# Kernel optimization log

Hardware: AMD Instinct MI355X
Metric: run time of the kernel (lower is better)

## Reference

```python
import jax, jax.numpy as jnp
import numpy as np

MAX_REL = 64  # max_relative_position (init kwarg)


def setup_inputs() -> dict:
    B, S, D, K = 8, 2048, 256, MAX_REL
    key = jax.random.key(0)
    ks = jax.random.split(key, 12)
    scale = 0.02
    return {
        "repre": jax.random.normal(ks[0], (B, S, D), jnp.float32),
        "mask": jnp.ones((B, S), jnp.int32),
        "wq1": jax.random.normal(ks[1], (D, D), jnp.float32) * scale,
        "bq1": jnp.zeros((D,), jnp.float32),
        "wk1": jax.random.normal(ks[2], (D, D), jnp.float32) * scale,
        "bk1": jnp.zeros((D,), jnp.float32),
        "rel1": jax.random.normal(ks[3], (2 * K + 1, D), jnp.float32) * scale,
        "wq2": jax.random.normal(ks[4], (D, D), jnp.float32) * scale,
        "bq2": jnp.zeros((D,), jnp.float32),
        "wk2": jax.random.normal(ks[5], (D, D), jnp.float32) * scale,
        "bk2": jnp.zeros((D,), jnp.float32),
        "rel2": jax.random.normal(ks[6], (2 * K + 1, D), jnp.float32) * scale,
    }


def _attn_logits(x, wq, bq, wk, bk, rel_emb, invalid, rel_idx):
    # Single-head relative-position attention scores (OpenNMT style):
    # query is pre-scaled by 1/sqrt(d); relative-key bias folded into scores.
    B, S, D = x.shape
    q = (x @ wq.T + bq) / jnp.sqrt(jnp.asarray(D, x.dtype))  # [B,S,D]
    k = x @ wk.T + bk                                        # [B,S,D]
    scores = jnp.einsum("bqd,bkd->bqk", q, k)               # [B,S,S]
    # relative-position term: q . rel_emb[clip(k-q)] without the [S,S,D] table
    q_rel = jnp.einsum("bqd,rd->bqr", q, rel_emb)            # [B,S,2K+1]
    idx = jnp.broadcast_to(rel_idx[None, :, :], (B, S, S))
    rel_scores = jnp.take_along_axis(q_rel, idx, axis=2)     # [B,S,S]
    scores = scores + rel_scores
    return jnp.where(invalid, jnp.asarray(-1e18, scores.dtype), scores)


def reference(repre, mask, wq1, bq1, wk1, bk1, rel1, wq2, bq2, wk2, bk2, rel2):
    B, S, D = repre.shape
    K = MAX_REL
    pos = jnp.arange(S)
    rel_idx = jnp.clip(pos[None, :] - pos[:, None], -K, K) + K  # [S,S] in [0,2K]
    # square_mask = ~(mask^T @ mask): attend only where both positions valid
    invalid = (mask[:, :, None] * mask[:, None, :]) == 0        # [B,S,S] bool
    span_st_logits = _attn_logits(repre, wq1, bq1, wk1, bk1, rel1, invalid, rel_idx)
    span_ed_logits = _attn_logits(repre, wq2, bq2, wk2, bk2, rel2, invalid, rel_idx)
    return (span_st_logits, span_ed_logits)
```

## Files before the change

### kernel.cpp

```cpp
#include <hip/hip_runtime.h>
#include <hip/hip_bf16.h>

typedef __attribute__((ext_vector_type(4))) float f32x4;
typedef __attribute__((ext_vector_type(8))) short short8;

#define BS   8
#define SQ   2048
#define DD   256
#define KREL 64
#define NREL 129

static const size_t OFF_XBF   = 0;
static const size_t OFF_WBF   = 8388608;
static const size_t OFF_RELBF = 8912896;
static const size_t OFF_WR    = 9044992;
static const size_t OFF_CR    = 9307136;
static const size_t OFF_QK    = 9309184;
static const size_t OFF_QR    = 42863616;

struct ConvArgs {
  const float* src[7];
  __hip_bfloat16* dst[7];
  float scale[7];
  int cum4[8];
};
struct bf4 { __hip_bfloat16 a, b, c, d; };

__global__ __launch_bounds__(256) void convert_k(ConvArgs A) {
  const int idx = blockIdx.x * 256 + threadIdx.x;
  if (idx >= A.cum4[7]) return;
  int rg = 0;
  #pragma unroll
  for (int t = 1; t < 7; ++t) rg += (idx >= A.cum4[t]);
  const int local = idx - A.cum4[rg];
  const float4 v = ((const float4*)A.src[rg])[local];
  const float sc = A.scale[rg];
  bf4 o;
  o.a = __float2bfloat16(v.x * sc);
  o.b = __float2bfloat16(v.y * sc);
  o.c = __float2bfloat16(v.z * sc);
  o.d = __float2bfloat16(v.w * sc);
  ((bf4*)A.dst[rg])[local] = o;
}

__global__ __launch_bounds__(256) void wr_k(const __hip_bfloat16* __restrict__ relbf,
                                            const __hip_bfloat16* __restrict__ wbf,
                                            const float* __restrict__ bq1,
                                            const float* __restrict__ bq2,
                                            __hip_bfloat16* __restrict__ wr,
                                            float* __restrict__ cr) {
  const int r = blockIdx.x;
  const int h = blockIdx.y;
  const int e = threadIdx.x;
  const int lane = e & 63, wv = e >> 6;
  const __hip_bfloat16* rel = relbf + (size_t)h * (NREL * DD);
  const __hip_bfloat16* wq  = wbf + (size_t)h * (2 * DD * DD);
  float a0 = 0.f, a1 = 0.f, a2 = 0.f, a3 = 0.f;
  if (r < NREL) {
    #pragma unroll 4
    for (int d = 0; d < DD; d += 4) {
      a0 += __bfloat162float(rel[r * DD + d + 0]) * __bfloat162float(wq[(d + 0) * DD + e]);
      a1 += __bfloat162float(rel[r * DD + d + 1]) * __bfloat162float(wq[(d + 1) * DD + e]);
      a2 += __bfloat162float(rel[r * DD + d + 2]) * __bfloat162float(wq[(d + 2) * DD + e]);
      a3 += __bfloat162float(rel[r * DD + d + 3]) * __bfloat162float(wq[(d + 3) * DD + e]);
    }
  }
  wr[((size_t)h * DD + r) * DD + e] = __float2bfloat16((a0 + a1) + (a2 + a3));

  const float* bq = h ? bq2 : bq1;
  float p = (r < NREL) ? bq[e] * 0.0625f * __bfloat162float(rel[r * DD + e]) : 0.f;
  #pragma unroll
  for (int o = 32; o > 0; o >>= 1) p += __shfl_down(p, o, 64);
  __shared__ float wred[4];
  if (lane == 0) wred[wv] = p;
  __syncthreads();
  if (e == 0) cr[h * DD + r] = (wred[0] + wred[1]) + (wred[2] + wred[3]);
}

__device__ __forceinline__ void stage_tile(const __hip_bfloat16* __restrict__ A,
                                           const __hip_bfloat16* __restrict__ B,
                                           int rowBase, int colBase, int k0,
                                           char* As, char* Bs, int wv, int lane) {
  #pragma unroll
  for (int inst = 0; inst < 2; ++inst) {
    const int lds_off = wv * 2048 + inst * 1024;
    const int e0 = (lds_off >> 1) + lane * 8;
    const int r  = e0 >> 5;
    const int kk = e0 & 31;
    __builtin_amdgcn_global_load_lds(
        (const __attribute__((address_space(1))) void*)(A + (size_t)(rowBase + r) * DD + k0 + kk),
        (__attribute__((address_space(3))) void*)(As + lds_off), 16, 0, 0);
    __builtin_amdgcn_global_load_lds(
        (const __attribute__((address_space(1))) void*)(B + (size_t)(colBase + r) * DD + k0 + kk),
        (__attribute__((address_space(3))) void*)(Bs + lds_off), 16, 0, 0);
  }
}

__device__ __forceinline__ void gemm_dbuf(const __hip_bfloat16* __restrict__ A,
                                          const __hip_bfloat16* __restrict__ B,
                                          int rowBase, int colBase,
                                          char* lds,
                                          f32x4 acc[4][4]) {
  const int tid  = threadIdx.x;
  const int lane = tid & 63;
  const int wv   = tid >> 6;
  const int wrow = (wv >> 1) * 64;
  const int wcol = (wv & 1) * 64;
  const int m    = lane & 15;
  const int quad = lane >> 4;

  char* As[2] = {lds, lds + 16384};
  char* Bs[2] = {lds + 8192, lds + 24576};

  const f32x4 zf = {0.f, 0.f, 0.f, 0.f};
  #pragma unroll
  for (int si = 0; si < 4; ++si)
    #pragma unroll
    for (int sj = 0; sj < 4; ++sj) acc[si][sj] = zf;

  stage_tile(A, B, rowBase, colBase, 0, As[0], Bs[0], wv, lane);
  __syncthreads();

  #pragma unroll
  for (int k = 0; k < 8; ++k) {
    const int cur = k & 1, nxt = cur ^ 1;
    if (k < 7)
      stage_tile(A, B, rowBase, colBase, (k + 1) * 32, As[nxt], Bs[nxt], wv, lane);

    short8 af[4], bf[4];
    #pragma unroll
    for (int s = 0; s < 4; ++s) {
      af[s] = *(const short8*)(As[cur] + (wrow + s * 16 + m) * 64 + quad * 16);
      bf[s] = *(const short8*)(Bs[cur] + (wcol + s * 16 + m) * 64 + quad * 16);
    }
    #pragma unroll
    for (int si = 0; si < 4; ++si)
      #pragma unroll
      for (int sj = 0; sj < 4; ++sj)
        acc[si][sj] = __builtin_amdgcn_mfma_f32_16x16x32_bf16(af[si], bf[sj], acc[si][sj], 0, 0, 0);
    __syncthreads();
  }
}

struct QKArgs {
  const __hip_bfloat16* X;
  const __hip_bfloat16* W[6];
  const float* bias[6];
  void* out[6];
  float bscale[6];
  int isf32[6];
};

__global__ __launch_bounds__(256) void qk_k(QKArgs A) {
  __shared__ char lds[32768];
  const int z = blockIdx.z;
  const int rowBase = blockIdx.y * 128;
  const int colBase = blockIdx.x * 128;
  f32x4 acc[4][4];
  gemm_dbuf(A.X, A.W[z], rowBase, colBase, lds, acc);

  const int tid  = threadIdx.x;
  const int lane = tid & 63;
  const int wv   = tid >> 6;
  const int wrow = (wv >> 1) * 64;
  const int wcol = (wv & 1) * 64;
  const int m    = lane & 15;
  const int quad = lane >> 4;

  const float* bias = A.bias[z];
  const float bs = A.bscale[z];
  const int f32o = A.isf32[z];
  float* fo = (float*)A.out[z];
  __hip_bfloat16* bo = (__hip_bfloat16*)A.out[z];

  #pragma unroll
  for (int sj = 0; sj < 4; ++sj) {
    const int j = colBase + wcol + sj * 16 + m;
    const float bj = bias[j] * bs;
    #pragma unroll
    for (int si = 0; si < 4; ++si) {
      const int i0 = rowBase + wrow + si * 16 + quad * 4;
      #pragma unroll
      for (int r = 0; r < 4; ++r) {
        const float v = acc[si][sj][r] + bj;
        const size_t idx = (size_t)(i0 + r) * DD + j;
        if (f32o) fo[idx] = v;
        else      bo[idx] = __float2bfloat16(v);
      }
    }
  }
}

__global__ __launch_bounds__(256) void score_k(const __hip_bfloat16* __restrict__ Q1,
                                               const __hip_bfloat16* __restrict__ K1,
                                               const float* __restrict__ QR1,
                                               const __hip_bfloat16* __restrict__ Q2,
                                               const __hip_bfloat16* __restrict__ K2,
                                               const float* __restrict__ QR2,
                                               const int* __restrict__ mask,
                                               float* __restrict__ out) {
  __shared__ char lds[32768];
  const int z = blockIdx.z;
  const int h = z >> 3, b = z & 7;
  const __hip_bfloat16* Q  = (h ? Q2 : Q1) + (size_t)b * SQ * DD;
  const __hip_bfloat16* Kk = (h ? K2 : K1) + (size_t)b * SQ * DD;
  const float* QR = (h ? QR2 : QR1) + (size_t)b * SQ * DD;
  const int* mk = mask + b * SQ;
  float* outp = out + (size_t)z * SQ * SQ;
  const int rowBase = blockIdx.y * 128;
  const int colBase = blockIdx.x * 128;

  f32x4 acc[4][4];
  gemm_dbuf(Q, Kk, rowBase, colBase, lds, acc);

  const int tid  = threadIdx.x;
  const int lane = tid & 63;
  const int wv   = tid >> 6;
  const int wrow = (wv >> 1) * 64;
  const int wcol = (wv & 1) * 64;
  const int m    = lane & 15;
  const int quad = lane >> 4;

  int mjv[4];
  #pragma unroll
  for (int sj = 0; sj < 4; ++sj) mjv[sj] = mk[colBase + wcol + sj * 16 + m];

  #pragma unroll
  for (int si = 0; si < 4; ++si) {
    #pragma unroll
    for (int r = 0; r < 4; ++r) {
      const int i = rowBase + wrow + si * 16 + quad * 4 + r;
      const int mi = mk[i];
      const float* qr_row = QR + (size_t)i * DD;
      float* orow = outp + (size_t)i * SQ;
      #pragma unroll
      for (int sj = 0; sj < 4; ++sj) {
        const int j = colBase + wcol + sj * 16 + m;
        int d = j - i;
        d = d < -KREL ? -KREL : (d > KREL ? KREL : d);
        float v = acc[si][sj][r] + qr_row[d + KREL];
        if (!(mi && mjv[sj])) v = -1e18f;
        orow[j] = v;
      }
    }
  }
}

extern "C" void kernel_launch(void* const* d_in, const int* in_sizes, int n_in,
                              void* d_out, int out_size, void* d_ws, size_t ws_size,
                              hipStream_t stream) {
  const float* repre = (const float*)d_in[0];
  const int*   mask  = (const int*)d_in[1];
  const float* wq1 = (const float*)d_in[2];
  const float* bq1 = (const float*)d_in[3];
  const float* wk1 = (const float*)d_in[4];
  const float* bk1 = (const float*)d_in[5];
  const float* rel1 = (const float*)d_in[6];
  const float* wq2 = (const float*)d_in[7];
  const float* bq2 = (const float*)d_in[8];
  const float* wk2 = (const float*)d_in[9];
  const float* bk2 = (const float*)d_in[10];
  const float* rel2 = (const float*)d_in[11];

  char* ws = (char*)d_ws;
  __hip_bfloat16* xbf   = (__hip_bfloat16*)(ws + OFF_XBF);
  __hip_bfloat16* wbf   = (__hip_bfloat16*)(ws + OFF_WBF);
  __hip_bfloat16* relbf = (__hip_bfloat16*)(ws + OFF_RELBF);
  __hip_bfloat16* wr    = (__hip_bfloat16*)(ws + OFF_WR);
  float*          cr    = (float*)(ws + OFF_CR);
  __hip_bfloat16* Q1 = (__hip_bfloat16*)(ws + OFF_QK);
  __hip_bfloat16* K1 = Q1 + (size_t)16384 * 256;
  __hip_bfloat16* Q2 = K1 + (size_t)16384 * 256;
  __hip_bfloat16* K2 = Q2 + (size_t)16384 * 256;
  float* QR1 = (float*)(ws + OFF_QR);
  float* QR2 = QR1 + (size_t)16384 * 256;

  ConvArgs ca;
  ca.src[0] = repre; ca.dst[0] = xbf;            ca.scale[0] = 1.f;
  ca.src[1] = wq1;   ca.dst[1] = wbf;            ca.scale[1] = 0.0625f;
  ca.src[2] = wk1;   ca.dst[2] = wbf + 65536;    ca.scale[2] = 1.f;
  ca.src[3] = wq2;   ca.dst[3] = wbf + 131072;   ca.scale[3] = 0.0625f;
  ca.src[4] = wk2;   ca.dst[4] = wbf + 196608;   ca.scale[4] = 1.f;
  ca.src[5] = rel1;  ca.dst[5] = relbf;          ca.scale[5] = 1.f;
  ca.src[6] = rel2;  ca.dst[6] = relbf + 33024;  ca.scale[6] = 1.f;
  const int sizes[7] = {4194304, 65536, 65536, 65536, 65536, 33024, 33024};
  int cum = 0;
  ca.cum4[0] = 0;
  for (int i = 0; i < 7; ++i) { cum += sizes[i] / 4; ca.cum4[i + 1] = cum; }
  const int nblk = (cum + 255) / 256;
  hipLaunchKernelGGL(convert_k, dim3(nblk), dim3(256), 0, stream, ca);

  hipLaunchKernelGGL(wr_k, dim3(256, 2), dim3(256), 0, stream, relbf, wbf, bq1, bq2, wr, cr);

  QKArgs qa;
  qa.X = xbf;
  qa.W[0] = wbf;          qa.bias[0] = bq1;      qa.bscale[0] = 0.0625f; qa.out[0] = Q1;  qa.isf32[0] = 0;
  qa.W[1] = wbf + 65536;  qa.bias[1] = bk1;      qa.bscale[1] = 1.f;     qa.out[1] = K1;  qa.isf32[1] = 0;
  qa.W[2] = wr;           qa.bias[2] = cr;       qa.bscale[2] = 1.f;     qa.out[2] = QR1; qa.isf32[2] = 1;
  qa.W[3] = wbf + 131072; qa.bias[3] = bq2;      qa.bscale[3] = 0.0625f; qa.out[3] = Q2;  qa.isf32[3] = 0;
  qa.W[4] = wbf + 196608; qa.bias[4] = bk2;      qa.bscale[4] = 1.f;     qa.out[4] = K2;  qa.isf32[4] = 0;
  qa.W[5] = wr + 65536;   qa.bias[5] = cr + 256; qa.bscale[5] = 1.f;     qa.out[5] = QR2; qa.isf32[5] = 1;
  hipLaunchKernelGGL(qk_k, dim3(2, 128, 6), dim3(256), 0, stream, qa);

  hipLaunchKernelGGL(score_k, dim3(16, 16, 16), dim3(256), 0, stream,
                     Q1, K1, QR1, Q2, K2, QR2, mask, (float*)d_out);
}
```

Baseline: 474.9 us.

## Transpose MFMA output layout for vectorized epilogue stores and skip clipped rel lookups

Swaps the MFMA operand order so each lane holds four consecutive columns of one row. The QK and score epilogues can then write 16-byte (fp32) or 8-byte (bf16) vector stores, and bias and mask are read as vectors. In score tiles that lie entirely beyond the relative window, one clipped rel value per row is used instead of a per-element gather. The aim is to cut the many scalar stores in the store-bound output of about 268 MB; the cost is more branch logic in the epilogue.

```diff
diff --git a/kernel.cpp b/kernel.cpp
--- a/kernel.cpp
+++ b/kernel.cpp
@@ -3,6 +3,8 @@
 
 typedef __attribute__((ext_vector_type(4))) float f32x4;
 typedef __attribute__((ext_vector_type(8))) short short8;
+
+struct bf16x4 { __hip_bfloat16 a, b, c, d; };
 
 #define BS   8
 #define SQ   2048
@@ -137,7 +139,7 @@
     for (int si = 0; si < 4; ++si)
       #pragma unroll
       for (int sj = 0; sj < 4; ++sj)
-        acc[si][sj] = __builtin_amdgcn_mfma_f32_16x16x32_bf16(af[si], bf[sj], acc[si][sj], 0, 0, 0);
+        acc[si][sj] = __builtin_amdgcn_mfma_f32_16x16x32_bf16(bf[sj], af[si], acc[si][sj], 0, 0, 0);
     __syncthreads();
   }
 }
@@ -174,18 +176,25 @@
   __hip_bfloat16* bo = (__hip_bfloat16*)A.out[z];
 
   #pragma unroll
-  for (int sj = 0; sj < 4; ++sj) {
-    const int j = colBase + wcol + sj * 16 + m;
-    const float bj = bias[j] * bs;
-    #pragma unroll
-    for (int si = 0; si < 4; ++si) {
-      const int i0 = rowBase + wrow + si * 16 + quad * 4;
+  for (int si = 0; si < 4; ++si) {
+    const int i = rowBase + wrow + si * 16 + m;
+    #pragma unroll
+    for (int sj = 0; sj < 4; ++sj) {
+      const int j0 = colBase + wcol + sj * 16 + quad * 4;
+      const f32x4 bj = *(const f32x4*)(bias + j0);
+      f32x4 v;
       #pragma unroll
-      for (int r = 0; r < 4; ++r) {
-        const float v = acc[si][sj][r] + bj;
-        const size_t idx = (size_t)(i0 + r) * DD + j;
-        if (f32o) fo[idx] = v;
-        else      bo[idx] = __float2bfloat16(v);
+      for (int r = 0; r < 4; ++r) v[r] = acc[si][sj][r] + bj[r] * bs;
+      const size_t idx = (size_t)i * DD + j0;
+      if (f32o) {
+        *(f32x4*)(fo + idx) = v;
+      } else {
+        bf16x4 o;
+        o.a = __float2bfloat16(v[0]);
+        o.b = __float2bfloat16(v[1]);
+        o.c = __float2bfloat16(v[2]);
+        o.d = __float2bfloat16(v[3]);
+        *(bf16x4*)(bo + idx) = o;
       }
     }
   }
@@ -221,27 +230,43 @@
   const int m    = lane & 15;
   const int quad = lane >> 4;
 
-  int mjv[4];
-  #pragma unroll
-  for (int sj = 0; sj < 4; ++sj) mjv[sj] = mk[colBase + wcol + sj * 16 + m];
+  const int delta = colBase - rowBase;
+  const int mode = (delta >= 192) ? 1 : (delta <= -192 ? -1 : 0);
+
+  int4 mj4[4];
+  #pragma unroll
+  for (int sj = 0; sj < 4; ++sj)
+    mj4[sj] = *(const int4*)(mk + colBase + wcol + sj * 16 + quad * 4);
 
   #pragma unroll
   for (int si = 0; si < 4; ++si) {
-    #pragma unroll
-    for (int r = 0; r < 4; ++r) {
-      const int i = rowBase + wrow + si * 16 + quad * 4 + r;
-      const int mi = mk[i];
-      const float* qr_row = QR + (size_t)i * DD;
-      float* orow = outp + (size_t)i * SQ;
-      #pragma unroll
-      for (int sj = 0; sj < 4; ++sj) {
-        const int j = colBase + wcol + sj * 16 + m;
-        int d = j - i;
-        d = d < -KREL ? -KREL : (d > KREL ? KREL : d);
-        float v = acc[si][sj][r] + qr_row[d + KREL];
-        if (!(mi && mjv[sj])) v = -1e18f;
-        orow[j] = v;
+    const int i = rowBase + wrow + si * 16 + m;
+    const int mi = mk[i];
+    const float* qr_row = QR + (size_t)i * DD;
+    float* orow = outp + (size_t)i * SQ;
+    float relc = 0.f;
+    if (mode) relc = qr_row[mode == 1 ? 2 * KREL : 0];
+    #pragma unroll
+    for (int sj = 0; sj < 4; ++sj) {
+      const int j0 = colBase + wcol + sj * 16 + quad * 4;
+      f32x4 v;
+      if (mode) {
+        #pragma unroll
+        for (int r = 0; r < 4; ++r) v[r] = acc[si][sj][r] + relc;
+      } else {
+        #pragma unroll
+        for (int r = 0; r < 4; ++r) {
+          int d = j0 + r - i;
+          d = d < -KREL ? -KREL : (d > KREL ? KREL : d);
+          v[r] = acc[si][sj][r] + qr_row[d + KREL];
+        }
       }
+      const int4 mj = mj4[sj];
+      if (!(mi && mj.x)) v[0] = -1e18f;
+      if (!(mi && mj.y)) v[1] = -1e18f;
+      if (!(mi && mj.z)) v[2] = -1e18f;
+      if (!(mi && mj.w)) v[3] = -1e18f;
+      *(f32x4*)(orow + j0) = v;
     }
   }
 }
```

Measured after the change: 415.4 us. 12.5% less time.
